# Optimization experiments

Hardware: AMD Instinct MI355X
Metric: run time of the kernel (lower is better)

## Reference

```python
import jax, jax.numpy as jnp
import numpy as np

RADIUS = 2  # kernel_size=5 -> r = (5-1)//2
EPS = 1e-8


def _diff(x, r, axis):
    # sliding-window sum from a cumsum along `axis` (same trick as BoxFilter.diff_x/diff_y)
    def sl(a, b):
        idx = [slice(None)] * x.ndim
        idx[axis] = slice(a, b)
        return x[tuple(idx)]
    left = sl(r, 2 * r + 1)
    middle = sl(2 * r + 1, None) - sl(None, -2 * r - 1)
    right = sl(-1, None) - sl(-2 * r - 1, -r - 1)
    return jnp.concatenate([left, middle, right], axis=axis)


def box_filter(x, r):
    # cumsum over H then window-diff, cumsum over W then window-diff
    return _diff(_diff(jnp.cumsum(x, axis=2), r, 2).cumsum(axis=3), r, 3)


def resize_bilinear_align_corners(x, out_h, out_w):
    # x: [N, C, h, w] -> [N, C, out_h, out_w], align_corners=True
    n, c, h, w = x.shape
    ys = jnp.linspace(0.0, h - 1.0, out_h, dtype=x.dtype)
    xs = jnp.linspace(0.0, w - 1.0, out_w, dtype=x.dtype)
    y0 = jnp.floor(ys).astype(jnp.int32)
    x0 = jnp.floor(xs).astype(jnp.int32)
    y1 = jnp.minimum(y0 + 1, h - 1)
    x1 = jnp.minimum(x0 + 1, w - 1)
    wy = (ys - y0.astype(x.dtype))[None, None, :, None]
    wx = (xs - x0.astype(x.dtype))[None, None, None, :]
    rows = x[:, :, y0, :] * (1 - wy) + x[:, :, y1, :] * wy  # [N,C,out_h,w]
    out = rows[:, :, :, x0] * (1 - wx) + rows[:, :, :, x1] * wx
    return out


def setup_inputs() -> dict:
    key = jax.random.key(0)
    k1, k2, k3 = jax.random.split(key, 3)
    return {
        "input_lowres": jax.random.uniform(k1, (8, 3, 256, 256), dtype=jnp.float32),
        "guide_lowres": jax.random.uniform(k2, (8, 3, 256, 256), dtype=jnp.float32),
        "input_highres": jax.random.uniform(k3, (8, 3, 1024, 1024), dtype=jnp.float32),
    }


def reference(input_lowres, guide_lowres, input_highres):
    x_lr, y_lr, x_hr = input_lowres, guide_lowres, input_highres
    r = RADIUS
    _, _, h_lr, w_lr = x_lr.shape
    _, _, h_hr, w_hr = x_hr.shape
    N = box_filter(jnp.ones((1, 1, h_lr, w_lr), dtype=x_lr.dtype), r)  # window pixel counts
    mean_x = box_filter(x_lr, r) / N
    mean_y = box_filter(y_lr, r) / N
    cov_xy = box_filter(x_lr * y_lr, r) / N - mean_x * mean_y
    var_x = box_filter(x_lr * x_lr, r) / N - mean_x * mean_x
    A = cov_xy / (var_x + EPS)
    b = mean_y - A * mean_x
    mean_A = resize_bilinear_align_corners(A, h_hr, w_hr)
    mean_b = resize_bilinear_align_corners(b, h_hr, w_hr)
    return mean_A * x_hr + mean_b
```

## Files before the change

kernel.cpp:

```cpp
#include <hip/hip_runtime.h>


typedef float f4 __attribute__((ext_vector_type(4)));
typedef float f2 __attribute__((ext_vector_type(2)));

constexpr int H_LR = 256, W_LR = 256;
constexpr int H_HR = 1024, W_HR = 1024;
constexpr int NC   = 24;
constexpr int RAD  = 2;
constexpr int RPB  = 16;
constexpr int NAB  = 6;
constexpr int NST  = 10;
constexpr int CS_W = W_LR + 4;
constexpr int PD   = 8;

constexpr int LDS_BYTES = NAB * CS_W * 4 * 4;

__global__ void __launch_bounds__(256) fgf_fused(const float* __restrict__ xlr,
                                                 const float* __restrict__ ylr,
                                                 const float* __restrict__ xhr,
                                                 float* __restrict__ out) {
    __shared__ __align__(16) char lds[LDS_BYTES];
    auto sx = reinterpret_cast<float(*)[W_LR]>(lds);
    auto sy = reinterpret_cast<float(*)[W_LR]>(lds + NST * W_LR * 4);
    auto cs = reinterpret_cast<float(*)[CS_W][4]>(lds);
    auto ab = reinterpret_cast<f2(*)[W_LR]>(lds);

    const int c  = blockIdx.y;
    const int i0 = blockIdx.x * RPB;
    const int t  = (int)threadIdx.x;
    const float scale = (float)(H_LR - 1) / (float)(H_HR - 1);

    const int y0min = (int)((float)i0 * scale);

    const int lrbase = c * (H_LR * W_LR);
    f4  stv[5];
    int soff[5];
    #pragma unroll
    for (int r = 0; r < 5; ++r) {
        const int  idx = r * 256 + t;
        const bool isx = idx < NST * 64;
        const int  id2 = isx ? idx : idx - NST * 64;
        const int  lr  = id2 >> 6, q = id2 & 63;
        const int  gr  = y0min - 2 + lr;
        const float* src = isx ? xlr : ylr;
        f4 v = {0.f, 0.f, 0.f, 0.f};
        if (gr >= 0 && gr < H_LR) v = *(const f4*)(src + lrbase + gr * W_LR + q * 4);
        stv[r]  = v;
        soff[r] = (isx ? 0 : NST * W_LR) + lr * W_LR + q * 4;
    }
    {
        float* base = (float*)lds;
        #pragma unroll
        for (int r = 0; r < 5; ++r) *(f4*)(base + soff[r]) = stv[r];
    }
    __syncthreads();

    float vx[NST], vy[NST];
    #pragma unroll
    for (int l = 0; l < NST; ++l) { vx[l] = sx[l][t]; vy[l] = sy[l][t]; }
    __syncthreads();

    float pxy[NST], pxx[NST];
    #pragma unroll
    for (int l = 0; l < NST; ++l) { pxy[l] = vx[l] * vy[l]; pxx[l] = vx[l] * vx[l]; }
    float s0 = 0.f, s1 = 0.f, s2 = 0.f, s3 = 0.f;
    #pragma unroll
    for (int l = 0; l < 5; ++l) { s0 += vx[l]; s1 += vy[l]; s2 += pxy[l]; s3 += pxx[l]; }
    #pragma unroll
    for (int rr = 0; rr < NAB; ++rr) {
        const f4 v = {s0, s1, s2, s3};
        *(f4*)&cs[rr][t + 2][0] = v;
        if (rr + 1 < NAB) {
            s0 += vx[rr + 5] - vx[rr];
            s1 += vy[rr + 5] - vy[rr];
            s2 += pxy[rr + 5] - pxy[rr];
            s3 += pxx[rr + 5] - pxx[rr];
        }
    }
    if (t < 2) {
        const f4 z = {0.f, 0.f, 0.f, 0.f};
        #pragma unroll
        for (int rr = 0; rr < NAB; ++rr) {
            *(f4*)&cs[rr][t][0] = z;
            *(f4*)&cs[rr][t + W_LR + 2][0] = z;
        }
    }
    __syncthreads();

    const int hcnt = min(t + RAD, W_LR - 1) - max(t - RAD, 0) + 1;
    float aa[NAB], bb[NAB];
    #pragma unroll
    for (int rr = 0; rr < NAB; ++rr) {
        f4 s = {0.f, 0.f, 0.f, 0.f};
        #pragma unroll
        for (int d = 0; d < 5; ++d) s += *(const f4*)&cs[rr][t + d][0];
        const int r  = y0min + rr;
        const int v0 = max(r - RAD, 0), v1 = min(r + RAD, H_LR - 1);
        const float inv = 1.0f / (float)((v1 - v0 + 1) * hcnt);
        const float mx  = s.x * inv;
        const float my  = s.y * inv;
        const float cov = s.z * inv - mx * my;
        const float var = s.w * inv - mx * mx;
        aa[rr] = cov / (var + 1e-8f);
        bb[rr] = my - aa[rr] * mx;
    }
    __syncthreads();

    #pragma unroll
    for (int rr = 0; rr < NAB; ++rr) ab[rr][t] = f2{aa[rr], bb[rr]};
    __syncthreads();

    const int cl = max(t - 1, 0), ch = min(t + 1, W_LR - 1);
    f2 A3[NAB][3];
    #pragma unroll
    for (int rr = 0; rr < NAB; ++rr) {
        A3[rr][0] = ab[rr][cl];
        A3[rr][1] = ab[rr][t];
        A3[rr][2] = ab[rr][ch];
    }

    float wxv[4], wx0v[4];
    bool  lo[4], hi[4];
    #pragma unroll
    for (int m = 0; m < 4; ++m) {
        const int   j  = t * 4 + m;
        const float fx = (float)j * scale;
        const int   x0 = (int)fx;
        wxv[m]  = fx - (float)x0;
        wx0v[m] = 1.f - wxv[m];
        lo[m]   = (x0 < t);
        hi[m]   = (x0 == t) && (t < W_LR - 1);
    }

    const size_t hrbase = ((size_t)c << 20) + (size_t)i0 * W_HR + t * 4;
    const float* srcp = xhr + hrbase;
    float*       dstp = out + hrbase;

    f4 buf[PD];
    #pragma unroll
    for (int k = 0; k < PD; ++k)
        buf[k] = *(const f4*)(srcp + (size_t)k * W_HR);
    asm volatile("" ::: "memory");

    f2 c0l = A3[0][0], c0c = A3[0][1], c0r = A3[0][2];
    f2 c1l = A3[1][0], c1c = A3[1][1], c1r = A3[1][2];
    int cur = 0;

    #pragma unroll
    for (int k = 0; k < RPB; ++k) {
        const f4 xvk = buf[k & (PD - 1)];

        const float fy  = (float)(i0 + k) * scale;
        const int   yy0 = (int)fy;
        const int   l0  = yy0 - y0min;
        if (l0 != cur) {
            c0l = c1l; c0c = c1c; c0r = c1r;
            const int nxt = (l0 + 1 < NAB) ? l0 + 1 : NAB - 1;
            switch (nxt) {
                case 2:  c1l = A3[2][0]; c1c = A3[2][1]; c1r = A3[2][2]; break;
                case 3:  c1l = A3[3][0]; c1c = A3[3][1]; c1r = A3[3][2]; break;
                case 4:  c1l = A3[4][0]; c1c = A3[4][1]; c1r = A3[4][2]; break;
                default: c1l = A3[5][0]; c1c = A3[5][1]; c1r = A3[5][2]; break;
            }
            cur = l0;
        }
        const float wyk = (yy0 < H_LR - 1) ? (fy - (float)yy0) : 0.f;
        const float wy0 = 1.f - wyk;
        const f2 r0 = wy0 * c0l + wyk * c1l;
        const f2 r1 = wy0 * c0c + wyk * c1c;
        const f2 r2 = wy0 * c0r + wyk * c1r;

        f4 ov;
        #pragma unroll
        for (int m = 0; m < 4; ++m) {
            const f2 pl  = lo[m] ? r0 : r1;
            const f2 ph  = hi[m] ? r2 : r1;
            const f2 abv = wx0v[m] * pl + wxv[m] * ph;
            ov[m] = abv.x * xvk[m] + abv.y;
        }
        *(f4*)(dstp + (size_t)k * W_HR) = ov;

        if (k + PD < RPB) {
            buf[k & (PD - 1)] = *(const f4*)(srcp + (size_t)(k + PD) * W_HR);
            asm volatile("" ::: "memory");
        }
    }
}

extern "C" void kernel_launch(void* const* d_in, const int* in_sizes, int n_in,
                              void* d_out, int out_size, void* d_ws, size_t ws_size,
                              hipStream_t stream) {
    const float* x_lr = (const float*)d_in[0];
    const float* y_lr = (const float*)d_in[1];
    const float* x_hr = (const float*)d_in[2];
    float* out = (float*)d_out;

    dim3 grid(H_HR / RPB, NC, 1);
    fgf_fused<<<grid, 256, 0, stream>>>(x_lr, y_lr, x_hr, out);
}
```

Measured before the change: 41.10 us.

## Split fused guided filter into separate A/b coefficient kernel and streaming kernel

Replaces the single fused kernel with two launches. The first computes the low-res A and b coefficients once per row and channel into a workspace. The second streams the high-res image, loading six precomputed A/b rows from the workspace into LDS. This removes the fused version's redundant recomputation of overlapping box-filter rows in every block, and shrinks the streaming kernel's prologue before the high-res loads start. The cost is an extra kernel launch, a global round trip for the coefficients, and a serial dependency between the two kernels.

```diff
diff --git a/kernel.cpp b/kernel.cpp
--- a/kernel.cpp
+++ b/kernel.cpp
@@ -10,21 +10,67 @@
 constexpr int RAD  = 2;
 constexpr int RPB  = 16;
 constexpr int NAB  = 6;
-constexpr int NST  = 10;
 constexpr int CS_W = W_LR + 4;
 constexpr int PD   = 8;
 
-constexpr int LDS_BYTES = NAB * CS_W * 4 * 4;
+__global__ void __launch_bounds__(256) ab_kernel(const float* __restrict__ xlr,
+                                                 const float* __restrict__ ylr,
+                                                 f2* __restrict__ wsab) {
+    __shared__ float sx[5][W_LR];
+    __shared__ float sy[5][W_LR];
+    __shared__ __align__(16) float cs[CS_W][4];
 
-__global__ void __launch_bounds__(256) fgf_fused(const float* __restrict__ xlr,
-                                                 const float* __restrict__ ylr,
-                                                 const float* __restrict__ xhr,
-                                                 float* __restrict__ out) {
-    __shared__ __align__(16) char lds[LDS_BYTES];
-    auto sx = reinterpret_cast<float(*)[W_LR]>(lds);
-    auto sy = reinterpret_cast<float(*)[W_LR]>(lds + NST * W_LR * 4);
-    auto cs = reinterpret_cast<float(*)[CS_W][4]>(lds);
-    auto ab = reinterpret_cast<f2(*)[W_LR]>(lds);
+    const int r = blockIdx.x;
+    const int c = blockIdx.y;
+    const int t = (int)threadIdx.x;
+    const int lrbase = c * (H_LR * W_LR);
+
+    for (int idx = t; idx < 640; idx += 256) {
+        const bool isx = idx < 320;
+        const int  id2 = isx ? idx : idx - 320;
+        const int  lr  = id2 >> 6, q = id2 & 63;
+        const int  gr  = r - RAD + lr;
+        const float* src = isx ? xlr : ylr;
+        f4 v = {0.f, 0.f, 0.f, 0.f};
+        if (gr >= 0 && gr < H_LR) v = *(const f4*)(src + lrbase + gr * W_LR + q * 4);
+        if (isx) *(f4*)&sx[lr][q * 4] = v;
+        else     *(f4*)&sy[lr][q * 4] = v;
+    }
+    __syncthreads();
+
+    float s0 = 0.f, s1 = 0.f, s2 = 0.f, s3 = 0.f;
+    #pragma unroll
+    for (int l = 0; l < 5; ++l) {
+        const float vx = sx[l][t];
+        const float vy = sy[l][t];
+        s0 += vx; s1 += vy; s2 += vx * vy; s3 += vx * vx;
+    }
+    *(f4*)&cs[t + 2][0] = f4{s0, s1, s2, s3};
+    if (t < 2) {
+        const f4 z = {0.f, 0.f, 0.f, 0.f};
+        *(f4*)&cs[t][0] = z;
+        *(f4*)&cs[t + W_LR + 2][0] = z;
+    }
+    __syncthreads();
+
+    f4 s = {0.f, 0.f, 0.f, 0.f};
+    #pragma unroll
+    for (int d = 0; d < 5; ++d) s += *(const f4*)&cs[t + d][0];
+    const int  hcnt = min(t + RAD, W_LR - 1) - max(t - RAD, 0) + 1;
+    const int  vcnt = min(r + RAD, H_LR - 1) - max(r - RAD, 0) + 1;
+    const float inv = 1.0f / (float)(vcnt * hcnt);
+    const float mx  = s.x * inv;
+    const float my  = s.y * inv;
+    const float cov = s.z * inv - mx * my;
+    const float var = s.w * inv - mx * mx;
+    const float a   = cov / (var + 1e-8f);
+    wsab[(c << 16) | (r << 8) | t] = f2{a, my - a * mx};
+}
+
+__global__ void __launch_bounds__(256) fgf_stream(const f2* __restrict__ wsab,
+                                                  const float* __restrict__ xhr,
+                                                  float* __restrict__ out) {
+    __shared__ __align__(16) f2 ab2[NAB][W_LR];
 
     const int c  = blockIdx.y;
     const int i0 = blockIdx.x * RPB;
@@ -33,91 +79,26 @@
 
     const int y0min = (int)((float)i0 * scale);
 
-    const int lrbase = c * (H_LR * W_LR);
-    f4  stv[5];
-    int soff[5];
-    #pragma unroll
-    for (int r = 0; r < 5; ++r) {
-        const int  idx = r * 256 + t;
-        const bool isx = idx < NST * 64;
-        const int  id2 = isx ? idx : idx - NST * 64;
-        const int  lr  = id2 >> 6, q = id2 & 63;
-        const int  gr  = y0min - 2 + lr;
-        const float* src = isx ? xlr : ylr;
-        f4 v = {0.f, 0.f, 0.f, 0.f};
-        if (gr >= 0 && gr < H_LR) v = *(const f4*)(src + lrbase + gr * W_LR + q * 4);
-        stv[r]  = v;
-        soff[r] = (isx ? 0 : NST * W_LR) + lr * W_LR + q * 4;
-    }
     {
-        float* base = (float*)lds;
+        f4* dst = (f4*)&ab2[0][0];
         #pragma unroll
-        for (int r = 0; r < 5; ++r) *(f4*)(base + soff[r]) = stv[r];
-    }
-    __syncthreads();
-
-    float vx[NST], vy[NST];
-    #pragma unroll
-    for (int l = 0; l < NST; ++l) { vx[l] = sx[l][t]; vy[l] = sy[l][t]; }
-    __syncthreads();
-
-    float pxy[NST], pxx[NST];
-    #pragma unroll
-    for (int l = 0; l < NST; ++l) { pxy[l] = vx[l] * vy[l]; pxx[l] = vx[l] * vx[l]; }
-    float s0 = 0.f, s1 = 0.f, s2 = 0.f, s3 = 0.f;
-    #pragma unroll
-    for (int l = 0; l < 5; ++l) { s0 += vx[l]; s1 += vy[l]; s2 += pxy[l]; s3 += pxx[l]; }
-    #pragma unroll
-    for (int rr = 0; rr < NAB; ++rr) {
-        const f4 v = {s0, s1, s2, s3};
-        *(f4*)&cs[rr][t + 2][0] = v;
-        if (rr + 1 < NAB) {
-            s0 += vx[rr + 5] - vx[rr];
-            s1 += vy[rr + 5] - vy[rr];
-            s2 += pxy[rr + 5] - pxy[rr];
-            s3 += pxx[rr + 5] - pxx[rr];
+        for (int rnd = 0; rnd < 3; ++rnd) {
+            const int idx = rnd * 256 + t;
+            const int row = idx >> 7;
+            const int q   = idx & 127;
+            const int gr  = min(y0min + row, H_LR - 1);
+            dst[idx] = *(const f4*)((const float*)(wsab + ((c << 16) | (gr << 8))) + q * 4);
         }
     }
-    if (t < 2) {
-        const f4 z = {0.f, 0.f, 0.f, 0.f};
-        #pragma unroll
-        for (int rr = 0; rr < NAB; ++rr) {
-            *(f4*)&cs[rr][t][0] = z;
-            *(f4*)&cs[rr][t + W_LR + 2][0] = z;
-        }
-    }
-    __syncthreads();
-
-    const int hcnt = min(t + RAD, W_LR - 1) - max(t - RAD, 0) + 1;
-    float aa[NAB], bb[NAB];
-    #pragma unroll
-    for (int rr = 0; rr < NAB; ++rr) {
-        f4 s = {0.f, 0.f, 0.f, 0.f};
-        #pragma unroll
-        for (int d = 0; d < 5; ++d) s += *(const f4*)&cs[rr][t + d][0];
-        const int r  = y0min + rr;
-        const int v0 = max(r - RAD, 0), v1 = min(r + RAD, H_LR - 1);
-        const float inv = 1.0f / (float)((v1 - v0 + 1) * hcnt);
-        const float mx  = s.x * inv;
-        const float my  = s.y * inv;
-        const float cov = s.z * inv - mx * my;
-        const float var = s.w * inv - mx * mx;
-        aa[rr] = cov / (var + 1e-8f);
-        bb[rr] = my - aa[rr] * mx;
-    }
-    __syncthreads();
-
-    #pragma unroll
-    for (int rr = 0; rr < NAB; ++rr) ab[rr][t] = f2{aa[rr], bb[rr]};
     __syncthreads();
 
     const int cl = max(t - 1, 0), ch = min(t + 1, W_LR - 1);
     f2 A3[NAB][3];
     #pragma unroll
     for (int rr = 0; rr < NAB; ++rr) {
-        A3[rr][0] = ab[rr][cl];
-        A3[rr][1] = ab[rr][t];
-        A3[rr][2] = ab[rr][ch];
+        A3[rr][0] = ab2[rr][cl];
+        A3[rr][1] = ab2[rr][t];
+        A3[rr][2] = ab2[rr][ch];
     }
 
     float wxv[4], wx0v[4];
@@ -133,7 +114,7 @@
         hi[m]   = (x0 == t) && (t < W_LR - 1);
     }
 
-    const size_t hrbase = ((size_t)c << 20) + (size_t)i0 * W_HR + t * 4;
+    const size_t hrbase = ((size_t)c << 20) + (size_t)i0 * W_HR + (size_t)t * 4;
     const float* srcp = xhr + hrbase;
     float*       dstp = out + hrbase;
 
@@ -195,7 +176,11 @@
     const float* y_lr = (const float*)d_in[1];
     const float* x_hr = (const float*)d_in[2];
     float* out = (float*)d_out;
+    f2*    wsab = (f2*)d_ws;
 
-    dim3 grid(H_HR / RPB, NC, 1);
-    fgf_fused<<<grid, 256, 0, stream>>>(x_lr, y_lr, x_hr, out);
+    dim3 gA(H_LR, NC, 1);
+    ab_kernel<<<gA, 256, 0, stream>>>(x_lr, y_lr, wsab);
+
+    dim3 gB(H_HR / RPB, NC, 1);
+    fgf_stream<<<gB, 256, 0, stream>>>(wsab, x_hr, out);
 }
```

Result: slower. 51.26 us (+24.7%).
